# Performance work log

Measured on AMD Instinct MI355X. Metric: run time of the kernel, lower is better.

The kernel has to match this reference:

```python
import jax, jax.numpy as jnp
import numpy as np


def setup_inputs() -> dict:
    key = jax.random.key(0)
    k1, k2, k3, k4 = jax.random.split(key, 4)
    B, C, H, W = 8, 512, 64, 64  # h must equal w per the broadcast in the original
    opt = jax.random.normal(k1, (B, C, H, W), dtype=jnp.float32)
    sar = jax.random.normal(k2, (B, C, H, W), dtype=jnp.float32)
    # 1x1 conv weights, shape [out_c, in_c] (kernel spatial dims are 1x1)
    W_opt = jax.random.normal(k3, (C, C), dtype=jnp.float32) * (2.0 / C) ** 0.5
    W_sar = jax.random.normal(k4, (C, C), dtype=jnp.float32) * (2.0 / C) ** 0.5
    return {"opt": opt, "sar": sar, "W_opt": W_opt, "W_sar": W_sar}


def _branch(x, Wc):
    # 1x1 conv: per-pixel channel mixing. Q = K = V (same conv applied to same input).
    f = jnp.einsum('oc,bchw->bohw', Wc, x)            # (b,c,h,w)
    # S[b,c,i,j] = sum_h Q[b,c,h,i] * K[b,c,h,j]  (transpose(2,3) @ original)
    S = jnp.einsum('bchi,bchj->bcij', f, f)           # (b,c,w,w)
    # nn.Softmax() with no dim on 4D -> softmax over channel dim (axis=1)
    S = jax.nn.softmax(S, axis=1)
    return f, S


def reference(opt, sar, W_opt, W_sar):
    V_opt, S_opt = _branch(opt, W_opt)
    V_sar, S_sar = _branch(sar, W_sar)
    hadamard = S_opt * S_sar                          # (b,c,w,w); h==w lets it broadcast with V
    Att = (V_opt * hadamard) * (V_sar * hadamard)
    return Att
```

## Files before the change

kernel.cpp:

```cpp
#include <hip/hip_runtime.h>
#include <cstdint>

#define CCH 512
#define HW  4096
#define WDIM 64
#define NBATCH 8
#define CHW ((size_t)CCH * HW)

typedef __attribute__((ext_vector_type(8))) short bf16x8;
typedef __attribute__((ext_vector_type(4))) float f32x4;
typedef __attribute__((ext_vector_type(4))) unsigned u32x4;

__device__ __forceinline__ unsigned short f2bf(float x) {
  unsigned u = __float_as_uint(x);
  unsigned r = (u + 0x7FFFu + ((u >> 16) & 1u)) >> 16;
  return (unsigned short)r;
}
__device__ __forceinline__ float bf2f(unsigned short h) {
  return __uint_as_float(((unsigned)h) << 16);
}

__device__ __forceinline__ void gl_lds16(const void* g, void* l) {
  __builtin_amdgcn_global_load_lds(
      (const __attribute__((address_space(1))) void*)g,
      (__attribute__((address_space(3))) void*)l, 16, 0, 0);
}

__global__ __launch_bounds__(256) void wsplit_k(
    const float* __restrict__ Wo, const float* __restrict__ Wsr,
    unsigned short* __restrict__ Whl) {
  const int br = blockIdx.y;
  const float* W = br ? Wsr : Wo;
  const int i = blockIdx.x * 256 + threadIdx.x;
  const float x = W[i];
  const unsigned short h = f2bf(x);
  unsigned short* dst = Whl + (size_t)br * 524288;
  dst[i] = h;
  dst[262144 + i] = f2bf(x - bf2f(h));
}

__global__ __launch_bounds__(256, 4) void mfma_conv_k(
    const unsigned short* __restrict__ Whl,
    const float* __restrict__ opt, const float* __restrict__ sar,
    float* __restrict__ F, int b0) {
  const int z = blockIdx.z;
  const int br = z & 1, bl = z >> 1;
  const unsigned short* Ah_g = Whl + (size_t)br * 524288;
  const unsigned short* Al_g = Ah_g + 262144;
  const float* Xb = (br ? sar : opt) + (size_t)(b0 + bl) * CHW;
  const int n0 = blockIdx.x * 128, m0 = blockIdx.y * 128;

  __shared__ __align__(16) unsigned short Ahs[128 * 32];
  __shared__ __align__(16) unsigned short Als[128 * 32];
  __shared__ __align__(16) unsigned short Xhs[128 * 32];
  __shared__ __align__(16) unsigned short Xls[128 * 32];

  const int tid = threadIdx.x;
  const int wave = tid >> 6, lane = tid & 63;
  const int wn = wave * 32;

  f32x4 acc[8][2] = {};

  const int rl = lane >> 2;
  const int kcA = (((lane & 3) ^ ((lane >> 3) & 3)) * 8);

  const int n2 = lane * 2;
  const int kh = wave * 8;
  const int pX = (wave ^ ((n2 >> 1) & 3)) * 8;

  const int fr = lane & 15;
  const int khA = (((lane >> 4) ^ ((lane >> 1) & 3)) * 8);

  for (int k0 = 0; k0 < CCH; k0 += 32) {
    __syncthreads();
#pragma unroll
    for (int q = 0; q < 2; ++q) {
      const int rbase = wave * 32 + q * 16;
      const int r = rbase + rl;
      gl_lds16(Ah_g + (size_t)(m0 + r) * CCH + k0 + kcA, &Ahs[rbase * 32]);
      gl_lds16(Al_g + (size_t)(m0 + r) * CCH + k0 + kcA, &Als[rbase * 32]);
    }
    float2 xr[8];
#pragma unroll
    for (int s = 0; s < 8; ++s)
      xr[s] = *(const float2*)&Xb[(size_t)(k0 + kh + s) * HW + n0 + n2];

    u32x4 h0, h1, l0, l1;
#pragma unroll
    for (int w = 0; w < 4; ++w) {
      const unsigned ux0 = __float_as_uint(xr[2 * w].x);
      const unsigned ux1 = __float_as_uint(xr[2 * w + 1].x);
      const unsigned uy0 = __float_as_uint(xr[2 * w].y);
      const unsigned uy1 = __float_as_uint(xr[2 * w + 1].y);
      h0[w] = __builtin_amdgcn_perm(ux1, ux0, 0x07060302u);
      h1[w] = __builtin_amdgcn_perm(uy1, uy0, 0x07060302u);
      const float lx0 = xr[2 * w].x - __uint_as_float(ux0 & 0xFFFF0000u);
      const float lx1 = xr[2 * w + 1].x - __uint_as_float(ux1 & 0xFFFF0000u);
      const float ly0 = xr[2 * w].y - __uint_as_float(uy0 & 0xFFFF0000u);
      const float ly1 = xr[2 * w + 1].y - __uint_as_float(uy1 & 0xFFFF0000u);
      l0[w] = __builtin_amdgcn_perm(__float_as_uint(lx1), __float_as_uint(lx0),
                                    0x07060302u);
      l1[w] = __builtin_amdgcn_perm(__float_as_uint(ly1), __float_as_uint(ly0),
                                    0x07060302u);
    }
    *(u32x4*)&Xhs[n2 * 32 + pX] = h0;
    *(u32x4*)&Xhs[(n2 + 1) * 32 + pX] = h1;
    *(u32x4*)&Xls[n2 * 32 + pX] = l0;
    *(u32x4*)&Xls[(n2 + 1) * 32 + pX] = l1;

    __syncthreads();

    bf16x8 bh[2], bl2[2];
#pragma unroll
    for (int j = 0; j < 2; ++j) {
      const int n = wn + j * 16 + fr;
      bh[j] = *(const bf16x8*)&Xhs[n * 32 + khA];
      bl2[j] = *(const bf16x8*)&Xls[n * 32 + khA];
    }
#pragma unroll
    for (int i = 0; i < 8; ++i) {
      const bf16x8 ah = *(const bf16x8*)&Ahs[(i * 16 + fr) * 32 + khA];
      const bf16x8 al = *(const bf16x8*)&Als[(i * 16 + fr) * 32 + khA];
#pragma unroll
      for (int j = 0; j < 2; ++j) {
        acc[i][j] = __builtin_amdgcn_mfma_f32_16x16x32_bf16(ah, bh[j], acc[i][j], 0, 0, 0);
        acc[i][j] = __builtin_amdgcn_mfma_f32_16x16x32_bf16(ah, bl2[j], acc[i][j], 0, 0, 0);
        acc[i][j] = __builtin_amdgcn_mfma_f32_16x16x32_bf16(al, bh[j], acc[i][j], 0, 0, 0);
      }
    }
  }

  float* Fb = F + (size_t)z * CHW;
  const int col = lane & 15, rq = (lane >> 4) * 4;
#pragma unroll
  for (int i = 0; i < 8; ++i)
#pragma unroll
    for (int j = 0; j < 2; ++j) {
      const int n = n0 + wn + j * 16 + col;
#pragma unroll
      for (int r = 0; r < 4; ++r) {
        const int m = m0 + i * 16 + rq + r;
        Fb[(size_t)m * HW + n] = acc[i][j][r];
      }
    }
}

#define FT_S 72
__global__ __launch_bounds__(256, 4) void gram_k(
    const float* __restrict__ F, float* __restrict__ S) {
  const size_t base = ((size_t)blockIdx.y * CCH + blockIdx.x) * HW;
  const float* Fc = F + base;
  float* Sc = S + base;

  __shared__ float Fs[64 * 64];
  __shared__ unsigned short FtH[64 * FT_S];
  __shared__ unsigned short FtL[64 * FT_S];

  const int tid = threadIdx.x;
  const int wave = tid >> 6, lane = tid & 63;

#pragma unroll
  for (int t = 0; t < 4; ++t) {
    const int off = (wave * 4 + t) * 256;
    gl_lds16(Fc + off + lane * 4, &Fs[off]);
  }
  __syncthreads();

  {
    const int w = lane;
    const int hc = wave * 16;
    unsigned short hb[16], lb[16];
#pragma unroll
    for (int k = 0; k < 16; ++k) {
      const float x = Fs[(hc + k) * 64 + w];
      const unsigned short h = f2bf(x);
      hb[k] = h;
      lb[k] = f2bf(x - bf2f(h));
    }
    unsigned short* dh = &FtH[w * FT_S + hc];
    unsigned short* dl = &FtL[w * FT_S + hc];
    *(uint4*)(dh + 0) = *(uint4*)&hb[0];
    *(uint4*)(dh + 8) = *(uint4*)&hb[8];
    *(uint4*)(dl + 0) = *(uint4*)&lb[0];
    *(uint4*)(dl + 8) = *(uint4*)&lb[8];
  }
  __syncthreads();

  const int wm = (wave >> 1) * 32, wn = (wave & 1) * 32;
  const int fr = lane & 15, kq = (lane >> 4) * 8;

  f32x4 acc[2][2] = {};
#pragma unroll
  for (int kcc = 0; kcc < 2; ++kcc) {
    bf16x8 ah[2], al[2], bh[2], bl[2];
#pragma unroll
    for (int i = 0; i < 2; ++i) {
      ah[i] = *(const bf16x8*)&FtH[(wm + i * 16 + fr) * FT_S + kcc * 32 + kq];
      al[i] = *(const bf16x8*)&FtL[(wm + i * 16 + fr) * FT_S + kcc * 32 + kq];
      bh[i] = *(const bf16x8*)&FtH[(wn + i * 16 + fr) * FT_S + kcc * 32 + kq];
      bl[i] = *(const bf16x8*)&FtL[(wn + i * 16 + fr) * FT_S + kcc * 32 + kq];
    }
#pragma unroll
    for (int i = 0; i < 2; ++i)
#pragma unroll
      for (int j = 0; j < 2; ++j) {
        acc[i][j] = __builtin_amdgcn_mfma_f32_16x16x32_bf16(ah[i], bh[j], acc[i][j], 0, 0, 0);
        acc[i][j] = __builtin_amdgcn_mfma_f32_16x16x32_bf16(ah[i], bl[j], acc[i][j], 0, 0, 0);
        acc[i][j] = __builtin_amdgcn_mfma_f32_16x16x32_bf16(al[i], bh[j], acc[i][j], 0, 0, 0);
      }
  }

  const int rq = (lane >> 4) * 4;
#pragma unroll
  for (int i = 0; i < 2; ++i)
#pragma unroll
    for (int j = 0; j < 2; ++j) {
      const int n = wn + j * 16 + fr;
#pragma unroll
      for (int r = 0; r < 4; ++r) {
        const int m = wm + i * 16 + rq + r;
        Sc[m * 64 + n] = acc[i][j][r];
      }
    }
}

__global__ __launch_bounds__(1024, 4) void softmax_fuse_k(
    const float* __restrict__ S, const float* __restrict__ Fbuf,
    float* __restrict__ Out) {
  const int i = blockIdx.x;
  const int b = blockIdx.y;
  const int tid = threadIdx.x;
  const int jl = (tid & 15) * 4;
  const int g = tid >> 4;

  const size_t rowO = (size_t)(b * 2) * CHW + (size_t)i * WDIM;
  const size_t rowS = rowO + CHW;

  float4 xoc[8], xsc[8];
  float mo[4], lo[4], ms[4], ls[4];
#pragma unroll
  for (int k = 0; k < 4; ++k) { mo[k] = -1e30f; ms[k] = -1e30f; lo[k] = 0.f; ls[k] = 0.f; }

#pragma unroll
  for (int cc = 0; cc < 8; ++cc) {
    const int c = g * 8 + cc;
    const size_t off = (size_t)c * HW + jl;
    xoc[cc] = *(const float4*)&S[rowO + off];
    xsc[cc] = *(const float4*)&S[rowS + off];
    mo[0] = fmaxf(mo[0], xoc[cc].x); mo[1] = fmaxf(mo[1], xoc[cc].y);
    mo[2] = fmaxf(mo[2], xoc[cc].z); mo[3] = fmaxf(mo[3], xoc[cc].w);
    ms[0] = fmaxf(ms[0], xsc[cc].x); ms[1] = fmaxf(ms[1], xsc[cc].y);
    ms[2] = fmaxf(ms[2], xsc[cc].z); ms[3] = fmaxf(ms[3], xsc[cc].w);
  }
#pragma unroll
  for (int cc = 0; cc < 8; ++cc) {
    lo[0] += __expf(xoc[cc].x - mo[0]); lo[1] += __expf(xoc[cc].y - mo[1]);
    lo[2] += __expf(xoc[cc].z - mo[2]); lo[3] += __expf(xoc[cc].w - mo[3]);
    ls[0] += __expf(xsc[cc].x - ms[0]); ls[1] += __expf(xsc[cc].y - ms[1]);
    ls[2] += __expf(xsc[cc].z - ms[2]); ls[3] += __expf(xsc[cc].w - ms[3]);
  }

  __shared__ float sm[2][64][64];
  __shared__ float sl[2][64][64];
  __shared__ float Mf[2][64];
  __shared__ float Li[2][64];

  *(float4*)&sm[0][g][jl] = make_float4(mo[0], mo[1], mo[2], mo[3]);
  *(float4*)&sl[0][g][jl] = make_float4(lo[0], lo[1], lo[2], lo[3]);
  *(float4*)&sm[1][g][jl] = make_float4(ms[0], ms[1], ms[2], ms[3]);
  *(float4*)&sl[1][g][jl] = make_float4(ls[0], ls[1], ls[2], ls[3]);
  __syncthreads();

  if (tid < 128) {
    const int br = tid >> 6, j = tid & 63;
    float M = -1e30f;
#pragma unroll 16
    for (int t = 0; t < 64; ++t) M = fmaxf(M, sm[br][t][j]);
    float L = 0.f;
#pragma unroll 16
    for (int t = 0; t < 64; ++t) L += sl[br][t][j] * __expf(sm[br][t][j] - M);
    Mf[br][j] = M;
    Li[br][j] = 1.f / L;
  }
  __syncthreads();

  float4 Mo4 = *(const float4*)&Mf[0][jl];
  float4 iLo4 = *(const float4*)&Li[0][jl];
  float4 Ms4 = *(const float4*)&Mf[1][jl];
  float4 iLs4 = *(const float4*)&Li[1][jl];
  float Mov[4] = {Mo4.x, Mo4.y, Mo4.z, Mo4.w};
  float iLov[4] = {iLo4.x, iLo4.y, iLo4.z, iLo4.w};
  float Msv[4] = {Ms4.x, Ms4.y, Ms4.z, Ms4.w};
  float iLsv[4] = {iLs4.x, iLs4.y, iLs4.z, iLs4.w};

#pragma unroll
  for (int cc = 0; cc < 8; ++cc) {
    const int c = g * 8 + cc;
    const size_t off = (size_t)c * HW + jl;
    float4 fo = *(const float4*)&Fbuf[rowO + off];
    float4 fs = *(const float4*)&Fbuf[rowS + off];
    float xov[4] = {xoc[cc].x, xoc[cc].y, xoc[cc].z, xoc[cc].w};
    float xsv[4] = {xsc[cc].x, xsc[cc].y, xsc[cc].z, xsc[cc].w};
    float fov[4] = {fo.x, fo.y, fo.z, fo.w};
    float fsv[4] = {fs.x, fs.y, fs.z, fs.w};
    float ov[4];
#pragma unroll
    for (int k = 0; k < 4; ++k) {
      const float ho = __expf(xov[k] - Mov[k]) * iLov[k];
      const float hs = __expf(xsv[k] - Msv[k]) * iLsv[k];
      float h2 = ho * hs;
      h2 *= h2;
      ov[k] = fov[k] * fsv[k] * h2;
    }
    *(float4*)&Out[(size_t)b * CHW + (size_t)c * HW + (size_t)i * WDIM + jl] =
        make_float4(ov[0], ov[1], ov[2], ov[3]);
  }
}

extern "C" void kernel_launch(void* const* d_in, const int* in_sizes, int n_in,
                              void* d_out, int out_size, void* d_ws, size_t ws_size,
                              hipStream_t stream) {
  const float* opt = (const float*)d_in[0];
  const float* sar = (const float*)d_in[1];
  const float* Wo  = (const float*)d_in[2];
  const float* Wsr = (const float*)d_in[3];
  float* out = (float*)d_out;

  unsigned short* Whl = (unsigned short*)d_ws;
  const size_t whlElems = 2u * 2u * 262144u;
  const size_t perBl = 2 * CHW;
  const size_t perBlBytes = perBl * 8;
  int bc = (int)((ws_size - whlElems * 2) / perBlBytes);
  if (bc < 1) bc = 1;
  if (bc > NBATCH) bc = NBATCH;
  const int passes = (NBATCH + bc - 1) / bc;
  const int nbp = (NBATCH + passes - 1) / passes;

  float* Fbuf = (float*)(Whl + whlElems);
  float* Sbuf = Fbuf + (size_t)bc * perBl;

  hipLaunchKernelGGL(wsplit_k, dim3(1024, 2), dim3(256), 0, stream, Wo, Wsr, Whl);

  for (int b0 = 0; b0 < NBATCH; b0 += nbp) {
    const int nb = (NBATCH - b0 < nbp) ? (NBATCH - b0) : nbp;

    hipLaunchKernelGGL(mfma_conv_k, dim3(32, 4, nb * 2), dim3(256), 0, stream,
                       Whl, opt, sar, Fbuf, b0);

    hipLaunchKernelGGL(gram_k, dim3(CCH, nb * 2), dim3(256), 0, stream,
                       Fbuf, Sbuf);

    hipLaunchKernelGGL(softmax_fuse_k, dim3(WDIM, nb), dim3(1024), 0, stream,
                       Sbuf, Fbuf, out + (size_t)b0 * CHW);
  }
}
```

Measured before the change: 351.8 us.

## Double-buffer conv LDS tiles and switch waves to a 2x2 warp tiling

Reworks the 1x1-conv MFMA kernel to double-buffer the A (weight hi/lo) and X (input hi/lo) LDS tiles, so global loads for the next K-step overlap with MFMA work on the current one and only one barrier is needed per iteration. Waves now cover 64x64 sub-tiles in a 2x2 arrangement instead of 128x32 strips, which lowers LDS fragment reads per MFMA. X is loaded as scalar coalesced floats split into two 64-column halves. LDS use doubles and launch bounds drop to 2 blocks per CU, so occupancy falls in exchange for overlap.

New measurement: 409.0 us. 1.16x slower.

```diff
diff --git a/kernel.cpp b/kernel.cpp
--- a/kernel.cpp
+++ b/kernel.cpp
@@ -39,7 +39,7 @@
   dst[262144 + i] = f2bf(x - bf2f(h));
 }
 
-__global__ __launch_bounds__(256, 4) void mfma_conv_k(
+__global__ __launch_bounds__(256, 2) void mfma_conv_k(
     const unsigned short* __restrict__ Whl,
     const float* __restrict__ opt, const float* __restrict__ sar,
     float* __restrict__ F, int b0) {
@@ -50,96 +50,121 @@
   const float* Xb = (br ? sar : opt) + (size_t)(b0 + bl) * CHW;
   const int n0 = blockIdx.x * 128, m0 = blockIdx.y * 128;
 
-  __shared__ __align__(16) unsigned short Ahs[128 * 32];
-  __shared__ __align__(16) unsigned short Als[128 * 32];
-  __shared__ __align__(16) unsigned short Xhs[128 * 32];
-  __shared__ __align__(16) unsigned short Xls[128 * 32];
+  __shared__ __align__(16) unsigned short Ahs[2][128 * 32];
+  __shared__ __align__(16) unsigned short Als[2][128 * 32];
+  __shared__ __align__(16) unsigned short Xhs[2][128 * 32];
+  __shared__ __align__(16) unsigned short Xls[2][128 * 32];
 
   const int tid = threadIdx.x;
   const int wave = tid >> 6, lane = tid & 63;
-  const int wn = wave * 32;
-
-  f32x4 acc[8][2] = {};
+  const int wm = (wave >> 1) * 64, wn = (wave & 1) * 64;
+
+  f32x4 acc[4][4] = {};
 
   const int rl = lane >> 2;
   const int kcA = (((lane & 3) ^ ((lane >> 3) & 3)) * 8);
 
-  const int n2 = lane * 2;
-  const int kh = wave * 8;
-  const int pX = (wave ^ ((n2 >> 1) & 3)) * 8;
+  const int rX = lane;
+  const int pX = (wave ^ ((lane >> 1) & 3)) * 8;
 
   const int fr = lane & 15;
-  const int khA = (((lane >> 4) ^ ((lane >> 1) & 3)) * 8);
-
-  for (int k0 = 0; k0 < CCH; k0 += 32) {
-    __syncthreads();
+  const int kq = (((lane >> 4) ^ ((lane >> 1) & 3)) * 8);
+
+  float xv[16];
+
+  auto stageA = [&](int k0, int cb) {
 #pragma unroll
     for (int q = 0; q < 2; ++q) {
       const int rbase = wave * 32 + q * 16;
       const int r = rbase + rl;
-      gl_lds16(Ah_g + (size_t)(m0 + r) * CCH + k0 + kcA, &Ahs[rbase * 32]);
-      gl_lds16(Al_g + (size_t)(m0 + r) * CCH + k0 + kcA, &Als[rbase * 32]);
-    }
-    float2 xr[8];
-#pragma unroll
-    for (int s = 0; s < 8; ++s)
-      xr[s] = *(const float2*)&Xb[(size_t)(k0 + kh + s) * HW + n0 + n2];
-
+      gl_lds16(Ah_g + (size_t)(m0 + r) * CCH + k0 + kcA, &Ahs[cb][rbase * 32]);
+      gl_lds16(Al_g + (size_t)(m0 + r) * CCH + k0 + kcA, &Als[cb][rbase * 32]);
+    }
+  };
+
+  auto loadX = [&](int k0) {
+#pragma unroll
+    for (int s = 0; s < 8; ++s) {
+      const size_t rowb = (size_t)(k0 + wave * 8 + s) * HW + n0;
+      xv[s] = Xb[rowb + rX];
+      xv[8 + s] = Xb[rowb + 64 + rX];
+    }
+  };
+
+  auto writeX = [&](int cb) {
     u32x4 h0, h1, l0, l1;
 #pragma unroll
     for (int w = 0; w < 4; ++w) {
-      const unsigned ux0 = __float_as_uint(xr[2 * w].x);
-      const unsigned ux1 = __float_as_uint(xr[2 * w + 1].x);
-      const unsigned uy0 = __float_as_uint(xr[2 * w].y);
-      const unsigned uy1 = __float_as_uint(xr[2 * w + 1].y);
-      h0[w] = __builtin_amdgcn_perm(ux1, ux0, 0x07060302u);
-      h1[w] = __builtin_amdgcn_perm(uy1, uy0, 0x07060302u);
-      const float lx0 = xr[2 * w].x - __uint_as_float(ux0 & 0xFFFF0000u);
-      const float lx1 = xr[2 * w + 1].x - __uint_as_float(ux1 & 0xFFFF0000u);
-      const float ly0 = xr[2 * w].y - __uint_as_float(uy0 & 0xFFFF0000u);
-      const float ly1 = xr[2 * w + 1].y - __uint_as_float(uy1 & 0xFFFF0000u);
-      l0[w] = __builtin_amdgcn_perm(__float_as_uint(lx1), __float_as_uint(lx0),
+      const unsigned a0 = __float_as_uint(xv[2 * w]);
+      const unsigned a1 = __float_as_uint(xv[2 * w + 1]);
+      const unsigned b0_ = __float_as_uint(xv[8 + 2 * w]);
+      const unsigned b1_ = __float_as_uint(xv[8 + 2 * w + 1]);
+      h0[w] = __builtin_amdgcn_perm(a1, a0, 0x07060302u);
+      h1[w] = __builtin_amdgcn_perm(b1_, b0_, 0x07060302u);
+      const float la0 = xv[2 * w] - __uint_as_float(a0 & 0xFFFF0000u);
+      const float la1 = xv[2 * w + 1] - __uint_as_float(a1 & 0xFFFF0000u);
+      const float lb0 = xv[8 + 2 * w] - __uint_as_float(b0_ & 0xFFFF0000u);
+      const float lb1 = xv[8 + 2 * w + 1] - __uint_as_float(b1_ & 0xFFFF0000u);
+      l0[w] = __builtin_amdgcn_perm(__float_as_uint(la1), __float_as_uint(la0),
                                     0x07060302u);
-      l1[w] = __builtin_amdgcn_perm(__float_as_uint(ly1), __float_as_uint(ly0),
+      l1[w] = __builtin_amdgcn_perm(__float_as_uint(lb1), __float_as_uint(lb0),
                                     0x07060302u);
     }
-    *(u32x4*)&Xhs[n2 * 32 + pX] = h0;
-    *(u32x4*)&Xhs[(n2 + 1) * 32 + pX] = h1;
-    *(u32x4*)&Xls[n2 * 32 + pX] = l0;
-    *(u32x4*)&Xls[(n2 + 1) * 32 + pX] = l1;
-
-    __syncthreads();
-
-    bf16x8 bh[2], bl2[2];
-#pragma unroll
-    for (int j = 0; j < 2; ++j) {
+    *(u32x4*)&Xhs[cb][rX * 32 + pX] = h0;
+    *(u32x4*)&Xhs[cb][(rX + 64) * 32 + pX] = h1;
+    *(u32x4*)&Xls[cb][rX * 32 + pX] = l0;
+    *(u32x4*)&Xls[cb][(rX + 64) * 32 + pX] = l1;
+  };
+
+  auto compute = [&](int cb) {
+    bf16x8 bh[4], blo[4];
+#pragma unroll
+    for (int j = 0; j < 4; ++j) {
       const int n = wn + j * 16 + fr;
-      bh[j] = *(const bf16x8*)&Xhs[n * 32 + khA];
-      bl2[j] = *(const bf16x8*)&Xls[n * 32 + khA];
-    }
-#pragma unroll
-    for (int i = 0; i < 8; ++i) {
-      const bf16x8 ah = *(const bf16x8*)&Ahs[(i * 16 + fr) * 32 + khA];
-      const bf16x8 al = *(const bf16x8*)&Als[(i * 16 + fr) * 32 + khA];
-#pragma unroll
-      for (int j = 0; j < 2; ++j) {
+      bh[j] = *(const bf16x8*)&Xhs[cb][n * 32 + kq];
+      blo[j] = *(const bf16x8*)&Xls[cb][n * 32 + kq];
+    }
+#pragma unroll
+    for (int i = 0; i < 4; ++i) {
+      const int m = wm + i * 16 + fr;
+      const bf16x8 ah = *(const bf16x8*)&Ahs[cb][m * 32 + kq];
+      const bf16x8 al = *(const bf16x8*)&Als[cb][m * 32 + kq];
+#pragma unroll
+      for (int j = 0; j < 4; ++j) {
         acc[i][j] = __builtin_amdgcn_mfma_f32_16x16x32_bf16(ah, bh[j], acc[i][j], 0, 0, 0);
-        acc[i][j] = __builtin_amdgcn_mfma_f32_16x16x32_bf16(ah, bl2[j], acc[i][j], 0, 0, 0);
+        acc[i][j] = __builtin_amdgcn_mfma_f32_16x16x32_bf16(ah, blo[j], acc[i][j], 0, 0, 0);
         acc[i][j] = __builtin_amdgcn_mfma_f32_16x16x32_bf16(al, bh[j], acc[i][j], 0, 0, 0);
       }
     }
-  }
+  };
+
+  stageA(0, 0);
+  loadX(0);
+  writeX(0);
+  __syncthreads();
+
+  int cur = 0;
+  for (int t = 0; t < 15; ++t) {
+    const int k0n = (t + 1) * 32;
+    stageA(k0n, cur ^ 1);
+    loadX(k0n);
+    compute(cur);
+    writeX(cur ^ 1);
+    __syncthreads();
+    cur ^= 1;
+  }
+  compute(cur);
 
   float* Fb = F + (size_t)z * CHW;
   const int col = lane & 15, rq = (lane >> 4) * 4;
 #pragma unroll
-  for (int i = 0; i < 8; ++i)
-#pragma unroll
-    for (int j = 0; j < 2; ++j) {
+  for (int i = 0; i < 4; ++i)
+#pragma unroll
+    for (int j = 0; j < 4; ++j) {
       const int n = n0 + wn + j * 16 + col;
 #pragma unroll
       for (int r = 0; r < 4; ++r) {
-        const int m = m0 + i * 16 + rq + r;
+        const int m = m0 + wm + i * 16 + rq + r;
         Fb[(size_t)m * HW + n] = acc[i][j][r];
       }
     }
```
